# Optimization experiments

Measured on AMD Instinct MI355X. Metric: run time of the kernel, lower is better.

The kernel has to match this reference:

```python
import jax, jax.numpy as jnp
import numpy as np
import math

B, L, D, H, ITEMS = 256, 200, 64, 2, 10000
HEAD = D // H
LN_EPS = 1e-12


def setup_inputs() -> dict:
    key = jax.random.key(0)
    ks = jax.random.split(key, 12)
    x = jax.random.normal(ks[0], (B, L, D), dtype=jnp.float32)
    attention_mask = jnp.zeros((B, L, L), dtype=jnp.float32)
    # distinct item ids per sequence -> well-conditioned C_sub submatrices
    perm_keys = jax.random.split(ks[1], B)
    seq_item_ids = jax.vmap(lambda k: jax.random.permutation(k, ITEMS)[:L])(perm_keys).astype(jnp.int32)
    # PSD-ish diversity kernel: C = 0.1 * F F^T + I  (guarantees invertible submatrices)
    F = jax.random.normal(ks[2], (ITEMS, 16), dtype=jnp.float32)
    C_kernel = 0.1 * (F @ F.T) + jnp.eye(ITEMS, dtype=jnp.float32)
    s = 1.0 / math.sqrt(D)
    Wq = jax.random.normal(ks[3], (D, D), dtype=jnp.float32) * s
    bq = jnp.zeros((D,), dtype=jnp.float32)
    Wv = jax.random.normal(ks[4], (D, D), dtype=jnp.float32) * s
    bv = jnp.zeros((D,), dtype=jnp.float32)
    Wd = jax.random.normal(ks[5], (D, D), dtype=jnp.float32) * s
    bd = jnp.zeros((D,), dtype=jnp.float32)
    ln_gamma = jnp.ones((D,), dtype=jnp.float32)
    ln_beta = jnp.zeros((D,), dtype=jnp.float32)
    return {"input_tensor": x, "attention_mask": attention_mask,
            "seq_item_ids": seq_item_ids, "C_kernel": C_kernel,
            "Wq": Wq, "bq": bq, "Wv": Wv, "bv": bv, "Wd": Wd, "bd": bd,
            "ln_gamma": ln_gamma, "ln_beta": ln_beta}


def _layer_norm(x, gamma, beta):
    mu = jnp.mean(x, axis=-1, keepdims=True)
    var = jnp.mean(jnp.square(x - mu), axis=-1, keepdims=True)
    return gamma * (x - mu) / jnp.sqrt(var + LN_EPS) + beta


def reference(input_tensor, attention_mask, seq_item_ids, C_kernel,
              Wq, bq, Wv, bv, Wd, bd, ln_gamma, ln_beta):
    x = input_tensor
    S = x @ Wq.T + bq                                    # [B,L,D]
    S2 = S * S
    L_kernel = jnp.einsum('bld,bmd->blm', S2, S2)        # [B,L,L]
    # gather per-sequence diversity submatrix C_sub[b,i,j] = C[ids[b,i], ids[b,j]]
    C_sub = C_kernel[seq_item_ids[:, :, None], seq_item_ids[:, None, :]]
    eye = jnp.eye(L, dtype=x.dtype)
    C_inv = jnp.linalg.inv(C_sub + 1e-4 * eye)
    T = jnp.einsum('blk,bkm->blm', L_kernel, C_inv)      # [B,L,L]
    diag_T = jnp.diagonal(T, axis1=1, axis2=2)           # [B,L]
    # 2x2 determinants of all (i,j) pairs: T_ii*T_jj - T_ij*T_ji
    subdet = diag_T[:, :, None] * diag_T[:, None, :] - T * jnp.swapaxes(T, 1, 2)
    triu = jnp.triu(jnp.ones((L, L), dtype=x.dtype), k=1)
    denom = jnp.sum(subdet * triu, axis=(1, 2), keepdims=True)
    denom = jnp.maximum(denom, 1e-9)
    subprob = subdet / denom
    diag_matrix = diag_T[:, :, None] * eye               # diag_embed
    score = -(subprob + diag_matrix) / math.sqrt(HEAD)
    score = score + attention_mask
    attn = jax.nn.softmax(score, axis=-1)
    V = x @ Wv.T + bv
    ctx = jnp.einsum('blm,bmd->bld', attn, V)
    out = ctx @ Wd.T + bd
    return _layer_norm(out + x, ln_gamma, ln_beta)
```

## Files before the change

kernel.cpp:

```cpp
#include <hip/hip_runtime.h>
#include <hip/hip_bf16.h>
#include <math.h>

#define NB 256
#define LL 200
#define DD 64
#define ITEMS_N 10000
#define RANK 16
#define ALPHA 1.0001f
#define INV_ALPHA (1.0f/1.0001f)
#define INV_SQRT_HEAD 0.17677669529663687f

typedef __attribute__((ext_vector_type(8))) short short8v;
typedef __attribute__((ext_vector_type(4))) float f32x4;

static __device__ __forceinline__ unsigned short f2b(float f) {
    unsigned u = __float_as_uint(f);
    unsigned r = (u + 0x7fffu + ((u >> 16) & 1u)) >> 16;
    return (unsigned short)r;
}
static __device__ __forceinline__ float b2f(unsigned short h) {
    return __uint_as_float(((unsigned)h) << 16);
}

#define OFF_A     0
#define OFF_TB    29952
#define OFF_CL32  (OFF_TB + 0)
#define OFF_U32   (OFF_TB + 4224)
#define OFF_UTL   (OFF_TB + 6400)
#define OFF_XB    (OFF_TB + 20000)
#define OFF_WQB   (OFF_TB + 49952)
#define OFF_WVB   (OFF_TB + 59168)
#define OFF_BQS   (OFF_TB + 68384)
#define OFF_BVS   (OFF_TB + 68640)
#define OFF_UL    126464
#define OFF_UB    139264
#define OFF_PB    145920
#define OFF_MAUG  (OFF_PB + 0)
#define OFF_IDSL  (OFF_PB + 2112)
#define OFF_PIV   (OFF_PB + 2912)
#define OFF_INVSQ (OFF_PB + 2976)
#define OFF_IDP   (OFF_PB + 3040)
#define OFF_ZB    152576
#define OFF_UTH   OFF_ZB
#define OFF_DV    159744
#define OFF_RED   160576
#define OFF_SCAL  160704
#define OFF_ZPAD  160720
#define LDS_TOTAL 160784

__global__ __launch_bounds__(1024) void mega_kernel(
        const float* __restrict__ x,    const float* __restrict__ mask,
        const int*   __restrict__ ids,  const float* __restrict__ C,
        const float* __restrict__ Wq,   const float* __restrict__ bq,
        const float* __restrict__ Wv,   const float* __restrict__ bv,
        const float* __restrict__ Wd,   const float* __restrict__ bd,
        const float* __restrict__ gamma,const float* __restrict__ beta,
        unsigned short* __restrict__ Vg, float* __restrict__ out) {
    extern __shared__ char smem[];
    unsigned short* Abuf = (unsigned short*)(smem + OFF_A);
    unsigned short* Tb   = (unsigned short*)(smem + OFF_TB);
    float* Cl32  = (float*)(smem + OFF_CL32);
    float* U32l  = (float*)(smem + OFF_U32);
    unsigned short* xbu  = (unsigned short*)(smem + OFF_XB);
    unsigned short* Wqbu = (unsigned short*)(smem + OFF_WQB);
    unsigned short* Wvbu = (unsigned short*)(smem + OFF_WVB);
    float* bqs   = (float*)(smem + OFF_BQS);
    float* bvs   = (float*)(smem + OFF_BVS);
    float*          Ul   = (float*)(smem + OFF_UL);
    unsigned short* Wdb  = (unsigned short*)(smem + OFF_UL);
    unsigned short* Ub   = (unsigned short*)(smem + OFF_UB);
    unsigned short* Pb   = (unsigned short*)(smem + OFF_PB);
    unsigned short* Zb   = (unsigned short*)(smem + OFF_ZB);
    float* dv   = (float*)(smem + OFF_DV);
    float* red  = (float*)(smem + OFF_RED);
    float* scal = (float*)(smem + OFF_SCAL);
    const short8v* zpad = (const short8v*)(smem + OFF_ZPAD);
    int*   idsl  = (int*)(smem + OFF_IDSL);
    int*   pivots= (int*)(smem + OFF_PIV);
    float* invsqv= (float*)(smem + OFF_INVSQ);
    int*   idpv  = (int*)(smem + OFF_IDP);
    float* Maug  = (float*)(smem + OFF_MAUG);

    int t = threadIdx.x;
    int b = blockIdx.x;
    int wv_ = t >> 6, lane = t & 63, fr = lane & 15, g = lane >> 4;

    int ga_ = t >> 5, gc_ = t & 31;
    float cgv;
    {
        int ia = ids[b*LL + ga_];
        int ic = ids[b*LL + gc_];
        cgv = C[(size_t)ia*ITEMS_N + ic];
    }

    {
        float4 z4; z4.x = 0.f; z4.y = 0.f; z4.z = 0.f; z4.w = 0.f;
        float4* tz = (float4*)(smem + OFF_TB + 92800);
        for (int i = t; i < 232; i += 1024) tz[i] = z4;
        float4* zz = (float4*)Zb;
        for (int i = t; i < 448; i += 1024) zz[i] = z4;
        if (t < 4) ((float4*)(smem + OFF_ZPAD))[t] = z4;
        if (t < 64)  ((unsigned*)(smem + OFF_UB + 6400))[t] = 0;
        if (t < 192) {
            int s = t / 12, c2 = t - s*12;
            *(unsigned*)(smem + OFF_UTL + s*448 + 400 + c2*4) = 0;
        }
        for (int i = t; i < 288; i += 1024) ((unsigned*)(smem + OFF_XB + 28800))[i] = 0;
        const float4* x4p = (const float4*)(x + (size_t)b*12800);
        #pragma unroll
        for (int it2 = 0; it2 < 4; ++it2) {
            int i4 = t + it2*1024;
            if (i4 < 3200) {
                float4 v4 = x4p[i4];
                int r = i4 >> 4, k4 = (i4 & 15) << 2;
                unsigned lo = (unsigned)f2b(v4.x) | ((unsigned)f2b(v4.y) << 16);
                unsigned hi = (unsigned)f2b(v4.z) | ((unsigned)f2b(v4.w) << 16);
                *(uint2*)(xbu + r*72 + k4) = make_uint2(lo, hi);
            }
        }
        {
            float4 q4 = ((const float4*)Wq)[t];
            float4 w4 = ((const float4*)Wv)[t];
            int d2 = t >> 4, k4 = (t & 15) << 2;
            unsigned qlo = (unsigned)f2b(q4.x) | ((unsigned)f2b(q4.y) << 16);
            unsigned qhi = (unsigned)f2b(q4.z) | ((unsigned)f2b(q4.w) << 16);
            *(uint2*)(Wqbu + d2*72 + k4) = make_uint2(qlo, qhi);
            unsigned vlo = (unsigned)f2b(w4.x) | ((unsigned)f2b(w4.y) << 16);
            unsigned vhi = (unsigned)f2b(w4.z) | ((unsigned)f2b(w4.w) << 16);
            *(uint2*)(Wvbu + d2*72 + k4) = make_uint2(vlo, vhi);
        }
        if (t < 64) { bqs[t] = bq[t]; bvs[t] = bv[t]; }
        if (t < LL) idsl[t] = ids[b*LL + t];
        Cl32[ga_*33 + gc_] = cgv;
    }
    __syncthreads();

    unsigned vpack[8];
    #pragma unroll
    for (int it2 = 0; it2 < 4; ++it2) {
        int tile = wv_ + 16*it2;
        vpack[2*it2] = 0; vpack[2*it2 + 1] = 0;
        if (tile < 52) {
            int R = tile >> 2, Dt = tile & 3;
            const char* ar = (const char*)smem + OFF_XB + (R*16 + fr)*144;
            const char* qr = (const char*)smem + OFF_WQB + (Dt*16 + fr)*144;
            const char* vr = (const char*)smem + OFF_WVB + (Dt*16 + fr)*144;
            short8v a0 = *(const short8v*)(ar + g*16);
            short8v a1 = *(const short8v*)(ar + 64 + g*16);
            f32x4 qa = {0.f,0.f,0.f,0.f};
            f32x4 va = {0.f,0.f,0.f,0.f};
            qa = __builtin_amdgcn_mfma_f32_16x16x32_bf16(a0, *(const short8v*)(qr + g*16), qa, 0,0,0);
            qa = __builtin_amdgcn_mfma_f32_16x16x32_bf16(a1, *(const short8v*)(qr + 64 + g*16), qa, 0,0,0);
            va = __builtin_amdgcn_mfma_f32_16x16x32_bf16(a0, *(const short8v*)(vr + g*16), va, 0,0,0);
            va = __builtin_amdgcn_mfma_f32_16x16x32_bf16(a1, *(const short8v*)(vr + 64 + g*16), va, 0,0,0);
            int col = Dt*16 + fr;
            float bqc = bqs[col], bvc = bvs[col];
            #pragma unroll
            for (int reg = 0; reg < 4; ++reg) {
                int row = R*16 + g*4 + reg;
                float sv = qa[reg] + bqc;
                Abuf[row*72 + col] = (row < LL) ? f2b(sv*sv) : (unsigned short)0;
            }
            vpack[2*it2]     = (unsigned)f2b(va[0] + bvc) | ((unsigned)f2b(va[1] + bvc) << 16);
            vpack[2*it2 + 1] = (unsigned)f2b(va[2] + bvc) | ((unsigned)f2b(va[3] + bvc) << 16);
        }
    }
    __syncthreads();

    if (wv_ == 0) {
        int a = lane & 31;
        float diag = Cl32[a*33 + a] - 1.0f;
        float ur[16];
        int   mypiv = 0; float myinv = 0.f;
        bool  removed = false;
        #pragma unroll
        for (int s = 0; s < RANK; ++s) {
            float v = removed ? -3e38f : diag;
            int idx = a;
            #pragma unroll
            for (int off = 16; off > 0; off >>= 1) {
                float v2 = __shfl_xor(v, off);
                int   i2 = __shfl_xor(idx, off);
                if (v2 > v || (v2 == v && i2 < idx)) { v = v2; idx = i2; }
            }
            int p = idx; float dp = v;
            float iv = (dp < 1e-9f) ? 0.0f : (1.0f/sqrtf(dp));
            float c = Cl32[a*33 + p] - ((a == p) ? 1.0f : 0.0f);
            #pragma unroll
            for (int k = 0; k < s; ++k) {
                float upk = __shfl(ur[k], p);
                c -= ur[k] * upk;
            }
            float u = c * iv;
            ur[s] = u;
            diag -= u*u;
            if (a == p) removed = true;
            if (lane == s) { mypiv = p; myinv = iv; }
        }
        #pragma unroll
        for (int s = 0; s < RANK; ++s) U32l[a*17 + s] = ur[s];
        if (lane < 16) {
            pivots[lane] = mypiv;
            invsqv[lane] = myinv;
            idpv[lane]   = idsl[mypiv];
        }
    } else {
        for (int idx = wv_ - 1; idx < 45; idx += 15) {
            int R = 2 + idx/13, Cc = idx % 13;
            short8v a0 = *(const short8v*)((char*)Abuf + (R*16 + fr)*144 + g*16);
            short8v a1 = *(const short8v*)((char*)Abuf + (R*16 + fr)*144 + 64 + g*16);
            short8v b0 = *(const short8v*)((char*)Abuf + (Cc*16 + fr)*144 + g*16);
            short8v b1 = *(const short8v*)((char*)Abuf + (Cc*16 + fr)*144 + 64 + g*16);
            f32x4 acc = {0.f, 0.f, 0.f, 0.f};
            acc = __builtin_amdgcn_mfma_f32_16x16x32_bf16(a0, b0, acc, 0, 0, 0);
            acc = __builtin_amdgcn_mfma_f32_16x16x32_bf16(a1, b1, acc, 0, 0, 0);
            int col = Cc*16 + fr;
            #pragma unroll
            for (int reg = 0; reg < 4; ++reg) {
                int row = R*16 + g*4 + reg;
                if (row < LL && col < LL) Tb[row*232 + col] = f2b(acc[reg]);
            }
        }
    }
    __syncthreads();

    if (wv_ < 4) {
        if (t < LL) {
            int myrow = idsl[t];
            float cg[16];
            #pragma unroll
            for (int s = 0; s < RANK; ++s)
                cg[s] = C[(size_t)myrow*ITEMS_N + idpv[s]];
            float ur[16];
            #pragma unroll
            for (int s = 0; s < RANK; ++s) {
                int p = pivots[s];
                float c = cg[s] - ((t == p) ? 1.0f : 0.0f);
                #pragma unroll
                for (int k = 0; k < s; ++k) c -= ur[k] * U32l[p*17 + k];
                ur[s] = c * invsqv[s];
            }
            unsigned short* Uth = (unsigned short*)(smem + OFF_UTH);
            unsigned short* Utl = (unsigned short*)(smem + OFF_UTL);
            #pragma unroll
            for (int s = 0; s < RANK; ++s) {
                float v = ur[s];
                Ul[t*RANK + s] = v;
                unsigned short hv = f2b(v);
                Ub[t*RANK + s] = hv;
                Uth[s*224 + t] = hv;
                Utl[s*224 + t] = f2b(v - b2f(hv));
            }
        }
    } else {
        for (int idx = 45 + (wv_ - 4); idx < 110; idx += 12) {
            int R = 2 + idx/13, Cc = idx % 13;
            short8v a0 = *(const short8v*)((char*)Abuf + (R*16 + fr)*144 + g*16);
            short8v a1 = *(const short8v*)((char*)Abuf + (R*16 + fr)*144 + 64 + g*16);
            short8v b0 = *(const short8v*)((char*)Abuf + (Cc*16 + fr)*144 + g*16);
            short8v b1 = *(const short8v*)((char*)Abuf + (Cc*16 + fr)*144 + 64 + g*16);
            f32x4 acc = {0.f, 0.f, 0.f, 0.f};
            acc = __builtin_amdgcn_mfma_f32_16x16x32_bf16(a0, b0, acc, 0, 0, 0);
            acc = __builtin_amdgcn_mfma_f32_16x16x32_bf16(a1, b1, acc, 0, 0, 0);
            int col = Cc*16 + fr;
            #pragma unroll
            for (int reg = 0; reg < 4; ++reg) {
                int row = R*16 + g*4 + reg;
                if (row < LL && col < LL) Tb[row*232 + col] = f2b(acc[reg]);
            }
        }
    }
    __syncthreads();

    if (wv_ == 0) {
        const char* uh  = smem + OFF_UTH;
        const char* ul2 = smem + OFF_UTL;
        f32x4 macc = {0.f,0.f,0.f,0.f};
        #pragma unroll
        for (int kb = 0; kb < 7; ++kb) {
            short8v h  = *(const short8v*)(uh  + fr*448 + kb*64 + g*16);
            short8v l2 = *(const short8v*)(ul2 + fr*448 + kb*64 + g*16);
            macc = __builtin_amdgcn_mfma_f32_16x16x32_bf16(h,  h,  macc, 0,0,0);
            macc = __builtin_amdgcn_mfma_f32_16x16x32_bf16(h,  l2, macc, 0,0,0);
            macc = __builtin_amdgcn_mfma_f32_16x16x32_bf16(l2, h,  macc, 0,0,0);
        }
        #pragma unroll
        for (int reg = 0; reg < 4; ++reg) {
            int r = g*4 + reg;
            Maug[r*33 + fr] = macc[reg] + ((r == fr) ? ALPHA : 0.f);
        }
        float m_[16], inv_[16];
        int rl = lane & 15;
        #pragma unroll
        for (int c = 0; c < 16; ++c) {
            m_[c]   = Maug[rl*33 + c];
            inv_[c] = (rl == c) ? 1.0f : 0.0f;
        }
        #pragma unroll
        for (int s = 0; s < 16; ++s) {
            float pv = __shfl(m_[s], s);
            float pvinv = 1.0f / pv;
            float f = m_[s];
            #pragma unroll
            for (int c = 0; c < 16; ++c) {
                float prow = __shfl(m_[c], s) * pvinv;
                float pinv = __shfl(inv_[c], s) * pvinv;
                if (lane == s) { m_[c] = prow; inv_[c] = pinv; }
                else { m_[c] = fmaf(-f, prow, m_[c]); inv_[c] = fmaf(-f, pinv, inv_[c]); }
            }
        }
        if (lane < 16) {
            #pragma unroll
            for (int c = 0; c < 16; ++c) Maug[lane*33 + 16 + c] = inv_[c];
        }
    } else {
        for (int i = t - 64; i < 2720; i += 960) {
            int r = 30 + (i >> 4), c2 = i & 15;
            *(unsigned*)(smem + OFF_TB + r*464 + 400 + c2*4) = 0;
        }
        for (int idx = 110 + (wv_ - 1); idx < 143; idx += 15) {
            int R = 2 + idx/13, Cc = idx % 13;
            short8v a0 = *(const short8v*)((char*)Abuf + (R*16 + fr)*144 + g*16);
            short8v a1 = *(const short8v*)((char*)Abuf + (R*16 + fr)*144 + 64 + g*16);
            short8v b0 = *(const short8v*)((char*)Abuf + (Cc*16 + fr)*144 + g*16);
            short8v b1 = *(const short8v*)((char*)Abuf + (Cc*16 + fr)*144 + 64 + g*16);
            f32x4 acc = {0.f, 0.f, 0.f, 0.f};
            acc = __builtin_amdgcn_mfma_f32_16x16x32_bf16(a0, b0, acc, 0, 0, 0);
            acc = __builtin_amdgcn_mfma_f32_16x16x32_bf16(a1, b1, acc, 0, 0, 0);
            int col = Cc*16 + fr;
            #pragma unroll
            for (int reg = 0; reg < 4; ++reg) {
                int row = R*16 + g*4 + reg;
                if (row < LL && col < LL) Tb[row*232 + col] = f2b(acc[reg]);
            }
        }
    }
    __syncthreads();

    for (int idx = t; idx < LL*RANK; idx += 1024) {
        int i = idx >> 4, r = idx & 15;
        float acc = 0.f;
        #pragma unroll
        for (int k = 0; k < 16; ++k) acc = fmaf(Ul[i*RANK + k], Maug[k*33 + 16 + r], acc);
        Zb[r*224 + i] = f2b(acc);
    }
    if (t < 480) {
        int r = t >> 4, c2 = t & 15;
        *(unsigned*)(smem + OFF_TB + r*464 + 400 + c2*4) = 0;
    }
    for (int u2 = wv_; u2 < 26; u2 += 16) {
        int R = u2 / 13, Cc = u2 - R*13;
        short8v a0 = *(const short8v*)((char*)Abuf + (R*16 + fr)*144 + g*16);
        short8v a1 = *(const short8v*)((char*)Abuf + (R*16 + fr)*144 + 64 + g*16);
        short8v b0 = *(const short8v*)((char*)Abuf + (Cc*16 + fr)*144 + g*16);
        short8v b1 = *(const short8v*)((char*)Abuf + (Cc*16 + fr)*144 + 64 + g*16);
        f32x4 acc = {0.f, 0.f, 0.f, 0.f};
        acc = __builtin_amdgcn_mfma_f32_16x16x32_bf16(a0, b0, acc, 0, 0, 0);
        acc = __builtin_amdgcn_mfma_f32_16x16x32_bf16(a1, b1, acc, 0, 0, 0);
        int col = Cc*16 + fr;
        #pragma unroll
        for (int reg = 0; reg < 4; ++reg) {
            int row = R*16 + g*4 + reg;
            if (row < LL && col < LL) Tb[row*232 + col] = f2b(acc[reg]);
        }
    }
    __syncthreads();

    {
        unsigned short* Vt = Abuf;
        #pragma unroll
        for (int it2 = 0; it2 < 4; ++it2) {
            int tile = wv_ + 16*it2;
            if (tile < 52) {
                int R = tile >> 2, Dt = tile & 3;
                #pragma unroll
                for (int reg = 0; reg < 4; ++reg) {
                    int row = R*16 + g*4 + reg;
                    if (row < LL) {
                        unsigned short hv = (unsigned short)
                            ((vpack[2*it2 + (reg >> 1)] >> ((reg & 1)*16)) & 0xffffu);
                        Vt[(Dt*16 + fr)*232 + row] = hv;
                    }
                }
            }
        }
        for (int i = t; i < 2048; i += 1024) {
            int d = i >> 5, mc = i & 31;
            Vt[d*232 + 200 + mc] = 0;
        }
        for (int i = t; i < 4096; i += 1024) {
            int dd = i >> 6, k = i & 63;
            Wdb[dd*72 + k] = f2b(Wd[i]);
        }
    }
    for (int strip = wv_; strip < 13; strip += 16) {
        f32x4 acc = {0.f, 0.f, 0.f, 0.f};
        const char* arow = (const char*)Tb + (size_t)(strip*16 + fr)*464;
        const char* brow = (const char*)Zb + (size_t)fr*448;
        #pragma unroll
        for (int kt = 0; kt < 7; ++kt) {
            short8v a  = *(const short8v*)(arow + kt*64 + g*16);
            short8v bb = *(const short8v*)(brow + kt*64 + g*16);
            acc = __builtin_amdgcn_mfma_f32_16x16x32_bf16(a, bb, acc, 0, 0, 0);
        }
        #pragma unroll
        for (int reg = 0; reg < 4; ++reg) {
            int prow = strip*16 + g*4 + reg;
            Pb[prow*16 + fr] = f2b(acc[reg]);
        }
    }
    __syncthreads();

    {
        float ps = 0.f, psd = 0.f;
        for (int u = wv_; u < 91; u += 16) {
            int R, Cc;
            if (u < 13) { R = u; Cc = u; }
            else {
                int q = u - 13, rr = 0;
                while (q >= 12 - rr) { q -= 12 - rr; ++rr; }
                R = rr; Cc = rr + 1 + q;
            }
            const short8v* pPR = (g < 2) ? (const short8v*)((const char*)Pb + (R*16 + fr)*32 + g*16) : zpad;
            const short8v* pUC = (g < 2) ? (const short8v*)((const char*)Ub + (Cc*16 + fr)*32 + g*16) : zpad;
            const short8v* pUR = (g < 2) ? (const short8v*)((const char*)Ub + (R*16 + fr)*32 + g*16) : zpad;
            const short8v* pPC = (g < 2) ? (const short8v*)((const char*)Pb + (Cc*16 + fr)*32 + g*16) : zpad;
            f32x4 acc1 = {0.f,0.f,0.f,0.f};
            f32x4 acc2 = {0.f,0.f,0.f,0.f};
            acc1 = __builtin_amdgcn_mfma_f32_16x16x32_bf16(*pPR, *pUC, acc1, 0,0,0);
            acc2 = __builtin_amdgcn_mfma_f32_16x16x32_bf16(*pUR, *pPC, acc2, 0,0,0);
            #pragma unroll
            for (int reg = 0; reg < 4; ++reg) {
                int row = R*16 + g*4 + reg, col = Cc*16 + fr;
                float lk = b2f(Tb[row*232 + col]);
                float tvA = (lk - acc1[reg]) * INV_ALPHA;
                float tvT = (lk - acc2[reg]) * INV_ALPHA;
                if (row < LL && col < LL) {
                    float w = tvA * tvT;
                    unsigned short h = f2b(w);
                    Tb[row*232 + col] = h;
                    if (u >= 13) {
                        Tb[col*232 + row] = h;
                        ps += 2.0f * w;
                    } else {
                        ps += w;
                        if (row == col) { dv[row] = tvA; psd += tvA; }
                    }
                }
            }
        }
        #pragma unroll
        for (int off = 32; off > 0; off >>= 1) {
            ps  += __shfl_xor(ps, off);
            psd += __shfl_xor(psd, off);
        }
        if (lane == 0) { red[wv_] = ps; red[16 + wv_] = psd; }
        __syncthreads();
        if (t == 0) {
            float s1 = 0.f, s2 = 0.f;
            for (int k = 0; k < 16; ++k) { s1 += red[k]; s2 += red[16 + k]; }
            float dn = fmaxf(0.5f*(s2*s2 - s1), 1e-9f);
            scal[0] = 1.0f / dn;
        }
        __syncthreads();
    }

    {
        const unsigned short* Vt = Abuf;
        float invden = scal[0];
        float bdv[4], gv[4], bev[4];
        #pragma unroll
        for (int d2 = 0; d2 < 4; ++d2) {
            bdv[d2] = bd[d2*16 + fr];
            gv[d2]  = gamma[d2*16 + fr];
            bev[d2] = beta[d2*16 + fr];
        }
        char* hb = smem + OFF_UB + wv_*1152;
        auto dorow = [&](const float (&mk)[13], int l) {
            if (l < LL) {
                float dl = dv[l];
                float sc[13]; float mx = -3e38f;
                #pragma unroll
                for (int e = 0; e < 13; ++e) {
                    int m = fr + 16*e;
                    if (m < LL) {
                        float wlm = b2f(Tb[l*232 + m]);
                        float sub = fmaf(dl, dv[m], -wlm);
                        float s = -(sub*invden + ((m == l) ? dl : 0.f))*INV_SQRT_HEAD
                                  + mk[e];
                        sc[e] = s; mx = fmaxf(mx, s);
                    } else sc[e] = -3e38f;
                }
                mx = fmaxf(mx, __shfl_xor(mx, 1));
                mx = fmaxf(mx, __shfl_xor(mx, 2));
                mx = fmaxf(mx, __shfl_xor(mx, 4));
                mx = fmaxf(mx, __shfl_xor(mx, 8));
                float sum = 0.f;
                #pragma unroll
                for (int e = 0; e < 13; ++e) {
                    int m = fr + 16*e;
                    float ev = (m < LL) ? __expf(sc[e] - mx) : 0.f;
                    sc[e] = ev; sum += ev;
                }
                sum += __shfl_xor(sum, 1);
                sum += __shfl_xor(sum, 2);
                sum += __shfl_xor(sum, 4);
                sum += __shfl_xor(sum, 8);
                float isum = 1.0f / sum;
                #pragma unroll
                for (int e = 0; e < 13; ++e) {
                    int m = fr + 16*e;
                    if (m < LL) Tb[l*232 + m] = f2b(sc[e]*isum);
                }
            }
        };
        for (int sp = wv_; sp < 13; sp += 16) {
            float mka0[13], mka1[13], mka2[13], mka3[13];
            {
                const float* mrow = mask + (size_t)b*40000 + (size_t)(sp*16 + g)*200;
                int l8 = sp*16 + g + 8;
                #pragma unroll
                for (int e = 0; e < 13; ++e) {
                    int m = fr + 16*e;
                    bool mm = (m < LL);
                    mka0[e] = mm                  ? mrow[m]        : 0.f;
                    mka1[e] = mm                  ? mrow[800 + m]  : 0.f;
                    mka2[e] = (mm && l8 < LL)     ? mrow[1600 + m] : 0.f;
                    mka3[e] = (mm && l8 + 4 < LL) ? mrow[2400 + m] : 0.f;
                }
            }
            dorow(mka0, sp*16 + g);
            dorow(mka1, sp*16 + 4 + g);
            dorow(mka2, sp*16 + 8 + g);
            dorow(mka3, sp*16 + 12 + g);
            float xp[16];
            #pragma unroll
            for (int d2 = 0; d2 < 4; ++d2)
                #pragma unroll
                for (int reg = 0; reg < 4; ++reg) {
                    int l = sp*16 + g*4 + reg;
                    xp[d2*4 + reg] = (l < LL)
                        ? x[((size_t)b*LL + l)*64 + d2*16 + fr] : 0.f;
                }
            f32x4 cacc[4];
            #pragma unroll
            for (int d2 = 0; d2 < 4; ++d2) { f32x4 z = {0.f,0.f,0.f,0.f}; cacc[d2] = z; }
            {
                const char* arow = (const char*)Tb + (size_t)(sp*16 + fr)*464;
                #pragma unroll
                for (int kt = 0; kt < 7; ++kt) {
                    short8v a = *(const short8v*)(arow + kt*64 + g*16);
                    #pragma unroll
                    for (int d2 = 0; d2 < 4; ++d2) {
                        short8v bb = *(const short8v*)((const char*)Vt + (d2*16 + fr)*464 + kt*64 + g*16);
                        cacc[d2] = __builtin_amdgcn_mfma_f32_16x16x32_bf16(a, bb, cacc[d2], 0, 0, 0);
                    }
                }
            }
            f32x4 oacc[4];
            #pragma unroll
            for (int d2 = 0; d2 < 4; ++d2) { f32x4 z = {0.f,0.f,0.f,0.f}; oacc[d2] = z; }
            #pragma unroll
            for (int h = 0; h < 2; ++h) {
                #pragma unroll
                for (int d2 = 0; d2 < 2; ++d2)
                    #pragma unroll
                    for (int reg = 0; reg < 4; ++reg)
                        *(unsigned short*)(hb + ((g*4 + reg)*36 + d2*16 + fr)*2) = f2b(cacc[h*2 + d2][reg]);
                short8v a = *(const short8v*)(hb + fr*72 + g*16);
                #pragma unroll
                for (int d2 = 0; d2 < 4; ++d2) {
                    short8v bb = *(const short8v*)((const char*)Wdb + (d2*16 + fr)*144 + h*64 + g*16);
                    oacc[d2] = __builtin_amdgcn_mfma_f32_16x16x32_bf16(a, bb, oacc[d2], 0, 0, 0);
                }
            }
            #pragma unroll
            for (int reg = 0; reg < 4; ++reg) {
                int l = sp*16 + g*4 + reg;
                if (l < LL) {
                    float z0 = oacc[0][reg] + bdv[0] + xp[reg];
                    float z1 = oacc[1][reg] + bdv[1] + xp[4 + reg];
                    float z2 = oacc[2][reg] + bdv[2] + xp[8 + reg];
                    float z3 = oacc[3][reg] + bdv[3] + xp[12 + reg];
                    float s = z0 + z1 + z2 + z3;
                    s += __shfl_xor(s, 1); s += __shfl_xor(s, 2);
                    s += __shfl_xor(s, 4); s += __shfl_xor(s, 8);
                    float mu = s * (1.0f/64.0f);
                    float c0 = z0 - mu, c1 = z1 - mu, c2 = z2 - mu, c3 = z3 - mu;
                    float vs = c0*c0 + c1*c1 + c2*c2 + c3*c3;
                    vs += __shfl_xor(vs, 1); vs += __shfl_xor(vs, 2);
                    vs += __shfl_xor(vs, 4); vs += __shfl_xor(vs, 8);
                    float rstd = rsqrtf(vs * (1.0f/64.0f) + 1e-12f);
                    float* op = out + ((size_t)b*LL + l)*64 + fr;
                    op[0]  = fmaf(gv[0]*rstd, c0, bev[0]);
                    op[16] = fmaf(gv[1]*rstd, c1, bev[1]);
                    op[32] = fmaf(gv[2]*rstd, c2, bev[2]);
                    op[48] = fmaf(gv[3]*rstd, c3, bev[3]);
                }
            }
        }
    }
}

extern "C" void kernel_launch(void* const* d_in, const int* in_sizes, int n_in,
                              void* d_out, int out_size, void* d_ws, size_t ws_size,
                              hipStream_t stream) {
    const float* x     = (const float*)d_in[0];
    const float* mask  = (const float*)d_in[1];
    const int*   ids   = (const int*)  d_in[2];
    const float* C     = (const float*)d_in[3];
    const float* Wq    = (const float*)d_in[4];
    const float* bq    = (const float*)d_in[5];
    const float* Wv    = (const float*)d_in[6];
    const float* bv    = (const float*)d_in[7];
    const float* Wd    = (const float*)d_in[8];
    const float* bd    = (const float*)d_in[9];
    const float* gamma = (const float*)d_in[10];
    const float* beta  = (const float*)d_in[11];
    float* out = (float*)d_out;

    unsigned short* Vb = (unsigned short*)d_ws;

    mega_kernel<<<NB, 1024, LDS_TOTAL, stream>>>(x, mask, ids, C, Wq, bq, Wv, bv,
                                                 Wd, bd, gamma, beta, Vb, out);
}
```

Measured before the change: 69.52 us.

## Prefetch attention-mask rows early and vectorize softmax over column pairs

Mask rows for the softmax stage are now loaded as float2 into registers at several earlier points, before the preceding barriers, so their global-memory latency overlaps with the inverse, T-matrix and V-transpose phases. The softmax loop now handles two adjacent columns per lane, using packed 32-bit LDS reads and writes of bf16 pairs and preloaded dv pairs. The small inverse is stored transposed in a separate LDS region for the Z computation. These loads are held live across phases, which raises register pressure, and the row-to-lane mapping inside each row changes.

```diff
diff --git a/kernel.cpp b/kernel.cpp
--- a/kernel.cpp
+++ b/kernel.cpp
@@ -37,10 +37,11 @@
 #define OFF_UB    139264
 #define OFF_PB    145920
 #define OFF_MAUG  (OFF_PB + 0)
-#define OFF_IDSL  (OFF_PB + 2112)
-#define OFF_PIV   (OFF_PB + 2912)
-#define OFF_INVSQ (OFF_PB + 2976)
-#define OFF_IDP   (OFF_PB + 3040)
+#define OFF_MINVT (OFF_PB + 2112)
+#define OFF_IDSL  (OFF_PB + 3392)
+#define OFF_PIV   (OFF_PB + 4192)
+#define OFF_INVSQ (OFF_PB + 4256)
+#define OFF_IDP   (OFF_PB + 4320)
 #define OFF_ZB    152576
 #define OFF_UTH   OFF_ZB
 #define OFF_DV    159744
@@ -81,6 +82,7 @@
     float* invsqv= (float*)(smem + OFF_INVSQ);
     int*   idpv  = (int*)(smem + OFF_IDP);
     float* Maug  = (float*)(smem + OFF_MAUG);
+    float* MinvT = (float*)(smem + OFF_MINVT);
 
     int t = threadIdx.x;
     int b = blockIdx.x;
@@ -312,7 +314,7 @@
         }
         if (lane < 16) {
             #pragma unroll
-            for (int c = 0; c < 16; ++c) Maug[lane*33 + 16 + c] = inv_[c];
+            for (int c = 0; c < 16; ++c) MinvT[c*20 + rl] = inv_[c];
         }
     } else {
         for (int i = t - 64; i < 2720; i += 960) {
@@ -338,11 +340,26 @@
     }
     __syncthreads();
 
+    float2 mk2a[7], mk2b[7];
+    {
+        int sp = wv_;
+        int l0 = sp*16 + g, l1 = sp*16 + 4 + g;
+        const float* mbase = mask + (size_t)b*40000;
+        #pragma unroll
+        for (int e = 0; e < 7; ++e) {
+            int m0 = 2*fr + 32*e;
+            bool mm = (sp < 13) && (m0 < LL);
+            mk2a[e] = (mm && l0 < LL) ? *(const float2*)(mbase + (size_t)l0*200 + m0)
+                                      : make_float2(0.f, 0.f);
+            mk2b[e] = (mm && l1 < LL) ? *(const float2*)(mbase + (size_t)l1*200 + m0)
+                                      : make_float2(0.f, 0.f);
+        }
+    }
     for (int idx = t; idx < LL*RANK; idx += 1024) {
         int i = idx >> 4, r = idx & 15;
         float acc = 0.f;
         #pragma unroll
-        for (int k = 0; k < 16; ++k) acc = fmaf(Ul[i*RANK + k], Maug[k*33 + 16 + r], acc);
+        for (int k = 0; k < 16; ++k) acc = fmaf(Ul[i*RANK + k], MinvT[r*20 + k], acc);
         Zb[r*224 + i] = f2b(acc);
     }
     if (t < 480) {
@@ -367,6 +384,18 @@
     }
     __syncthreads();
 
+    float2 mk2c[7];
+    {
+        int sp = wv_;
+        int l2 = sp*16 + 8 + g;
+        const float* mbase = mask + (size_t)b*40000;
+        #pragma unroll
+        for (int e = 0; e < 7; ++e) {
+            int m0 = 2*fr + 32*e;
+            mk2c[e] = ((sp < 13) && (m0 < LL) && (l2 < LL))
+                ? *(const float2*)(mbase + (size_t)l2*200 + m0) : make_float2(0.f, 0.f);
+        }
+    }
     {
         unsigned short* Vt = Abuf;
         #pragma unroll
@@ -412,6 +441,18 @@
     }
     __syncthreads();
 
+    float2 mk2d[7];
+    {
+        int sp = wv_;
+        int l3 = sp*16 + 12 + g;
+        const float* mbase = mask + (size_t)b*40000;
+        #pragma unroll
+        for (int e = 0; e < 7; ++e) {
+            int m0 = 2*fr + 32*e;
+            mk2d[e] = ((sp < 13) && (m0 < LL) && (l3 < LL))
+                ? *(const float2*)(mbase + (size_t)l3*200 + m0) : make_float2(0.f, 0.f);
+        }
+    }
     {
         float ps = 0.f, psd = 0.f;
         for (int u = wv_; u < 91; u += 16) {
@@ -469,71 +510,76 @@
     {
         const unsigned short* Vt = Abuf;
         float invden = scal[0];
-        float bdv[4], gv[4], bev[4];
-        #pragma unroll
-        for (int d2 = 0; d2 < 4; ++d2) {
-            bdv[d2] = bd[d2*16 + fr];
-            gv[d2]  = gamma[d2*16 + fr];
-            bev[d2] = beta[d2*16 + fr];
-        }
-        char* hb = smem + OFF_UB + wv_*1152;
-        auto dorow = [&](const float (&mk)[13], int l) {
-            if (l < LL) {
-                float dl = dv[l];
-                float sc[13]; float mx = -3e38f;
-                #pragma unroll
-                for (int e = 0; e < 13; ++e) {
-                    int m = fr + 16*e;
-                    if (m < LL) {
-                        float wlm = b2f(Tb[l*232 + m]);
-                        float sub = fmaf(dl, dv[m], -wlm);
-                        float s = -(sub*invden + ((m == l) ? dl : 0.f))*INV_SQRT_HEAD
-                                  + mk[e];
-                        sc[e] = s; mx = fmaxf(mx, s);
-                    } else sc[e] = -3e38f;
+        int sp = wv_;
+        if (sp < 13) {
+            float bdv[4], gv[4], bev[4];
+            #pragma unroll
+            for (int d2 = 0; d2 < 4; ++d2) {
+                bdv[d2] = bd[d2*16 + fr];
+                gv[d2]  = gamma[d2*16 + fr];
+                bev[d2] = beta[d2*16 + fr];
+            }
+            char* hb = smem + OFF_UB + wv_*1152;
+            float2 dvv[7];
+            #pragma unroll
+            for (int e = 0; e < 7; ++e) {
+                int m0 = 2*fr + 32*e;
+                dvv[e] = (m0 < LL) ? *(const float2*)(dv + m0) : make_float2(0.f, 0.f);
+            }
+            auto dorow = [&](const float2 (&mk)[7], int l) {
+                if (l < LL) {
+                    float dl = dv[l];
+                    float sc[14]; float mx = -3e38f;
+                    #pragma unroll
+                    for (int e = 0; e < 7; ++e) {
+                        int m0 = 2*fr + 32*e;
+                        if (m0 < LL) {
+                            unsigned w2 = *(const unsigned*)((const char*)Tb + ((size_t)l*232 + m0)*2);
+                            float w0 = b2f((unsigned short)(w2 & 0xffffu));
+                            float w1 = b2f((unsigned short)(w2 >> 16));
+                            float s0 = -(fmaf(dl, dvv[e].x, -w0)*invden
+                                         + ((m0 == l) ? dl : 0.f))*INV_SQRT_HEAD + mk[e].x;
+                            float s1 = -(fmaf(dl, dvv[e].y, -w1)*invden
+                                         + ((m0 + 1 == l) ? dl : 0.f))*INV_SQRT_HEAD + mk[e].y;
+                            sc[2*e] = s0; sc[2*e + 1] = s1;
+                            mx = fmaxf(mx, fmaxf(s0, s1));
+                        } else { sc[2*e] = -3e38f; sc[2*e + 1] = -3e38f; }
+                    }
+                    mx = fmaxf(mx, __shfl_xor(mx, 1));
+                    mx = fmaxf(mx, __shfl_xor(mx, 2));
+                    mx = fmaxf(mx, __shfl_xor(mx, 4));
+                    mx = fmaxf(mx, __shfl_xor(mx, 8));
+                    float sum = 0.f;
+                    #pragma unroll
+                    for (int e = 0; e < 7; ++e) {
+                        int m0 = 2*fr + 32*e;
+                        if (m0 < LL) {
+                            float e0 = __expf(sc[2*e] - mx);
+                            float e1 = __expf(sc[2*e + 1] - mx);
+                            sc[2*e] = e0; sc[2*e + 1] = e1;
+                            sum += e0 + e1;
+                        }
+                    }
+                    sum += __shfl_xor(sum, 1);
+                    sum += __shfl_xor(sum, 2);
+                    sum += __shfl_xor(sum, 4);
+                    sum += __shfl_xor(sum, 8);
+                    float isum = 1.0f / sum;
+                    #pragma unroll
+                    for (int e = 0; e < 7; ++e) {
+                        int m0 = 2*fr + 32*e;
+                        if (m0 < LL) {
+                            unsigned pw = (unsigned)f2b(sc[2*e]*isum)
+                                        | ((unsigned)f2b(sc[2*e + 1]*isum) << 16);
+                            *(unsigned*)((char*)Tb + ((size_t)l*232 + m0)*2) = pw;
+                        }
+                    }
                 }
-                mx = fmaxf(mx, __shfl_xor(mx, 1));
-                mx = fmaxf(mx, __shfl_xor(mx, 2));
-                mx = fmaxf(mx, __shfl_xor(mx, 4));
-                mx = fmaxf(mx, __shfl_xor(mx, 8));
-                float sum = 0.f;
-                #pragma unroll
-                for (int e = 0; e < 13; ++e) {
-                    int m = fr + 16*e;
-                    float ev = (m < LL) ? __expf(sc[e] - mx) : 0.f;
-                    sc[e] = ev; sum += ev;
-                }
-                sum += __shfl_xor(sum, 1);
-                sum += __shfl_xor(sum, 2);
-                sum += __shfl_xor(sum, 4);
-                sum += __shfl_xor(sum, 8);
-                float isum = 1.0f / sum;
-                #pragma unroll
-                for (int e = 0; e < 13; ++e) {
-                    int m = fr + 16*e;
-                    if (m < LL) Tb[l*232 + m] = f2b(sc[e]*isum);
-                }
-            }
-        };
-        for (int sp = wv_; sp < 13; sp += 16) {
-            float mka0[13], mka1[13], mka2[13], mka3[13];
-            {
-                const float* mrow = mask + (size_t)b*40000 + (size_t)(sp*16 + g)*200;
-                int l8 = sp*16 + g + 8;
-                #pragma unroll
-                for (int e = 0; e < 13; ++e) {
-                    int m = fr + 16*e;
-                    bool mm = (m < LL);
-                    mka0[e] = mm                  ? mrow[m]        : 0.f;
-                    mka1[e] = mm                  ? mrow[800 + m]  : 0.f;
-                    mka2[e] = (mm && l8 < LL)     ? mrow[1600 + m] : 0.f;
-                    mka3[e] = (mm && l8 + 4 < LL) ? mrow[2400 + m] : 0.f;
-                }
-            }
-            dorow(mka0, sp*16 + g);
-            dorow(mka1, sp*16 + 4 + g);
-            dorow(mka2, sp*16 + 8 + g);
-            dorow(mka3, sp*16 + 12 + g);
+            };
+            dorow(mk2a, sp*16 + g);
+            dorow(mk2b, sp*16 + 4 + g);
+            dorow(mk2c, sp*16 + 8 + g);
+            dorow(mk2d, sp*16 + 12 + g);
             float xp[16];
             #pragma unroll
             for (int d2 = 0; d2 < 4; ++d2)
```

New measurement: 70.46 us. Within noise of the previous version (+1.4%).
